# Kernel tuning notes

Measured on AMD Instinct MI355X. Metric: run time of the kernel, lower is better.

## Reference

```python
import jax, jax.numpy as jnp
import numpy as np

D = 256       # in_channels == hd_channels
H = 8         # heads
HC = D // H   # head dim = 32
NV = 30000    # variables
NC = 60000    # clauses
E = 120000    # edges per polarity


def setup_inputs() -> dict:
    key = jax.random.key(0)
    ks = jax.random.split(key, 16)
    std = 0.02
    v = jax.random.normal(ks[0], (NV, D), jnp.float32)
    c = jax.random.normal(ks[1], (NC, D), jnp.float32)
    # adj row0 indexes clauses (c), row1 indexes variables (v)
    adj_pos = jnp.stack([jax.random.randint(ks[2], (E,), 0, NC),
                         jax.random.randint(ks[3], (E,), 0, NV)]).astype(jnp.int32)
    adj_neg = jnp.stack([jax.random.randint(ks[4], (E,), 0, NC),
                         jax.random.randint(ks[5], (E,), 0, NV)]).astype(jnp.int32)
    # shared projections (ModuleList([lin]*2) shares one module)
    Wq = jax.random.normal(ks[6], (D, D), jnp.float32) * std
    bq = jnp.zeros((D,), jnp.float32)
    Wkv = jax.random.normal(ks[7], (D, 2 * D), jnp.float32) * std
    bkv = jnp.zeros((2 * D,), jnp.float32)
    ffn_v_w1 = jax.random.normal(ks[8], (D, D), jnp.float32) * std
    ffn_v_b1 = jnp.zeros((D,), jnp.float32)
    ffn_v_w2 = jax.random.normal(ks[9], (D, D), jnp.float32) * std
    ffn_v_b2 = jnp.zeros((D,), jnp.float32)
    ffn_c_w1 = jax.random.normal(ks[10], (D, D), jnp.float32) * std
    ffn_c_b1 = jnp.zeros((D,), jnp.float32)
    ffn_c_w2 = jax.random.normal(ks[11], (D, D), jnp.float32) * std
    ffn_c_b2 = jnp.zeros((D,), jnp.float32)
    ones = jnp.ones((D,), jnp.float32)
    zeros = jnp.zeros((D,), jnp.float32)
    return dict(v=v, c=c, adj_pos=adj_pos, adj_neg=adj_neg,
                Wq=Wq, bq=bq, Wkv=Wkv, bkv=bkv,
                ffn_v_w1=ffn_v_w1, ffn_v_b1=ffn_v_b1, ffn_v_w2=ffn_v_w2, ffn_v_b2=ffn_v_b2,
                ffn_c_w1=ffn_c_w1, ffn_c_b1=ffn_c_b1, ffn_c_w2=ffn_c_w2, ffn_c_b2=ffn_c_b2,
                ln_att_v_g=ones, ln_att_v_b=zeros, ln_ffn_v_g=ones, ln_ffn_v_b=zeros,
                ln_att_c_g=ones, ln_att_c_b=zeros, ln_ffn_c_g=ones, ln_ffn_c_b=zeros)


def _split(x):
    return x.reshape(x.shape[0], H, HC)


def _ln(x, g, b, eps=1e-5):
    m = jnp.mean(x, axis=-1, keepdims=True)
    va = jnp.mean(jnp.square(x - m), axis=-1, keepdims=True)
    return (x - m) * jax.lax.rsqrt(va + eps) * g + b


def _seg_softmax(x, seg, n):
    m = jax.ops.segment_max(x, seg, num_segments=n)      # (n, H)
    e = jnp.exp(x - m[seg])
    s = jax.ops.segment_sum(e, seg, num_segments=n)
    return e / s[seg]


def _sparse_attn(q, k, val, e_q, e_k, n_q):
    # q: (Lq,H,HC); k,val: (Lk,H,HC); per-edge dot -> segment softmax -> scatter aggregate
    qk = jnp.einsum('ehc,ehc->eh', q[e_q], k[e_k]) * (1.0 / np.sqrt(HC))
    alpha = _seg_softmax(qk, e_q, n_q)                   # (E,H)
    return jax.ops.segment_sum(alpha[:, :, None] * val[e_k], e_q, num_segments=n_q)


def _cross(x, y, adj, Wq, bq, Wkv, bkv):
    # adj[0] indexes y, adj[1] indexes x
    ey, ex = adj[0], adj[1]
    qx = _split(x @ Wq + bq)
    ky, vy = jnp.split(y @ Wkv + bkv, 2, axis=-1)
    w = _sparse_attn(qx, _split(ky), _split(vy), ex, ey, x.shape[0])   # x queries, transposed edges
    qy = _split(y @ Wq + bq)
    kx, vx = jnp.split(x @ Wkv + bkv, 2, axis=-1)
    u = _sparse_attn(qy, _split(kx), _split(vx), ey, ex, y.shape[0])   # y queries
    return w.reshape(x.shape[0], D), u.reshape(y.shape[0], D)


def _ffn(x, w1, b1, w2, b2):
    return jax.nn.gelu(x @ w1 + b1, approximate=False) @ w2 + b2


def reference(v, c, adj_pos, adj_neg, Wq, bq, Wkv, bkv,
              ffn_v_w1, ffn_v_b1, ffn_v_w2, ffn_v_b2,
              ffn_c_w1, ffn_c_b1, ffn_c_w2, ffn_c_b2,
              ln_att_v_g, ln_att_v_b, ln_ffn_v_g, ln_ffn_v_b,
              ln_att_c_g, ln_att_c_b, ln_ffn_c_g, ln_ffn_c_b):
    wp, up = _cross(v, c, adj_pos, Wq, bq, Wkv, bkv)
    wn, un = _cross(v, c, adj_neg, Wq, bq, Wkv, bkv)
    v1 = _ln(v + (wp + wn), ln_att_v_g, ln_att_v_b)
    c1 = _ln(c + (up + un), ln_att_c_g, ln_att_c_b)
    v2 = _ln(v1 + _ffn(v1, ffn_v_w1, ffn_v_b1, ffn_v_w2, ffn_v_b2), ln_ffn_v_g, ln_ffn_v_b)
    c2 = _ln(c1 + _ffn(c1, ffn_c_w1, ffn_c_b1, ffn_c_w2, ffn_c_b2), ln_ffn_c_g, ln_ffn_c_b)
    return (v2, c2)
```

## Files before the change

kernel.cpp:

```cpp
#include <hip/hip_runtime.h>
#include <math.h>

#define DD 256
#define NH 8

typedef __attribute__((ext_vector_type(8))) short short8;
typedef __attribute__((ext_vector_type(4))) float floatx4;

__device__ __forceinline__ float b2f(unsigned short u) {
    return __uint_as_float(((unsigned)u) << 16);
}
__device__ __forceinline__ unsigned short f2b(float f) {
    unsigned u = __float_as_uint(f);
    return (unsigned short)((u + 0x7fffu + ((u >> 16) & 1u)) >> 16);
}

__device__ __forceinline__ void gload_lds16(const void* g, void* l) {
    __builtin_amdgcn_global_load_lds(
        (const __attribute__((address_space(1))) void*)g,
        (__attribute__((address_space(3))) void*)l, 16, 0, 0);
}

__global__ void detect_dtype(const unsigned* __restrict__ ones_words, int* __restrict__ flag) {
    flag[0] = (ones_words[0] == 0x3F800000u) ? 0 : 1;
}

__device__ __forceinline__ void load8(const void* base, size_t off, int f32, unsigned short* dst) {
    if (f32) {
        const float4* p = (const float4*)((const float*)base + off);
        float4 x = p[0], y = p[1];
        dst[0] = f2b(x.x); dst[1] = f2b(x.y); dst[2] = f2b(x.z); dst[3] = f2b(x.w);
        dst[4] = f2b(y.x); dst[5] = f2b(y.y); dst[6] = f2b(y.z); dst[7] = f2b(y.w);
    } else {
        *(uint4*)dst = *(const uint4*)((const unsigned short*)base + off);
    }
}

__global__ void wt_build(const void* __restrict__ Wq, const void* __restrict__ Wkv,
                         const void* __restrict__ f1v, const void* __restrict__ f1c,
                         const void* __restrict__ f2v, const void* __restrict__ f2c,
                         short* __restrict__ wt, const int* __restrict__ flagp)
{
    const int extf = (*flagp == 0);
    const void* src; int N; size_t dst0;
    switch (blockIdx.z) {
        case 0:  src = Wq;  N = 256; dst0 = 0;          break;
        case 1:  src = Wkv; N = 512; dst0 = 256 * 256;  break;
        case 2:  src = f1v; N = 256; dst0 = 768 * 256;  break;
        case 3:  src = f1c; N = 256; dst0 = 1024 * 256; break;
        case 4:  src = f2v; N = 256; dst0 = 1280 * 256; break;
        default: src = f2c; N = 256; dst0 = 1536 * 256; break;
    }
    int n0 = blockIdx.x * 32, k0 = blockIdx.y * 32;
    if (n0 >= N) return;
    __shared__ short tile[32][33];
    int tx = threadIdx.x & 31, ty = threadIdx.x >> 5;
    #pragma unroll
    for (int i = 0; i < 32; i += 8) {
        int k = k0 + ty + i, n = n0 + tx;
        float val = extf ? ((const float*)src)[(size_t)k * N + n]
                         : b2f(((const unsigned short*)src)[(size_t)k * N + n]);
        tile[ty + i][tx] = (short)f2b(val);
    }
    __syncthreads();
    #pragma unroll
    for (int i = 0; i < 32; i += 8)
        wt[dst0 + (size_t)(n0 + ty + i) * 256 + k0 + tx] = tile[tx][ty + i];
}


__device__ __forceinline__ void stage_bchunk(const char* src32k, char* dst, int wave, int lane) {
    #pragma unroll
    for (int i = 0; i < 4; ++i) {
        int So = ((wave * 4 + i) << 10) + lane * 16;
        int Ls = So ^ (((So >> 9) & 7) << 4);
        gload_lds16(src32k + Ls, dst + ((wave * 4 + i) << 10));
    }
}

__device__ __forceinline__ short8 read_bfrag(const char* bbuf, int row, int bytecol) {
    int S = (row << 9) + bytecol;
    S ^= (row & 7) << 4;
    return *(const short8*)(bbuf + S);
}

__launch_bounds__(512)
__global__ void proj_gemm4(const void* __restrict__ va, const void* __restrict__ ca,
                           int NVr, int NCr, int bv,
                           const short* __restrict__ wt,
                           const void* __restrict__ bq, const void* __restrict__ bkv,
                           unsigned short* __restrict__ qbuf, unsigned short* __restrict__ kvbuf,
                           const int* __restrict__ flagp)
{
    __shared__ __align__(16) short As[128][264];
    __shared__ __align__(16) char Bs[2][64 * 512];
    const int extf = (*flagp == 0);
    const int t = threadIdx.x;
    const int wave = t >> 6, lane = t & 63;
    const int fr = lane & 15, fq = lane >> 4;
    const int bx = blockIdx.x;
    int grow0, nrows, abase_row; const void* asrc;
    if (bx < bv) { grow0 = bx * 128; asrc = va; abase_row = grow0; nrows = NVr - grow0; }
    else { int mc0 = (bx - bv) * 128; grow0 = NVr + mc0; asrc = ca; abase_row = mc0; nrows = NCr - mc0; }
    if (nrows > 128) nrows = 128;

    stage_bchunk((const char*)wt, Bs[0], wave, lane);
    {
        const int r = t >> 2, cb = (t & 3) * 8;
        #pragma unroll
        for (int cc = 0; cc < 8; ++cc) {
            int col = cb + cc * 32;
            __align__(16) unsigned short a8[8] = {0, 0, 0, 0, 0, 0, 0, 0};
            if (r < nrows) load8(asrc, (size_t)(abase_row + r) * DD + col, extf, a8);
            *(uint4*)(&As[r][col]) = *(const uint4*)a8;
        }
    }
    __syncthreads();

    int cur = 0;
    for (int nc = 0; nc < 12; ++nc) {
        if (nc + 1 < 12)
            stage_bchunk((const char*)(wt + (size_t)(nc + 1) * 64 * 256), Bs[cur ^ 1], wave, lane);
        floatx4 acc[4] = {};
        #pragma unroll
        for (int k8 = 0; k8 < 8; ++k8) {
            short8 af = *(const short8*)(&As[wave * 16 + fr][k8 * 32 + fq * 8]);
            short8 bf[4];
            #pragma unroll
            for (int j = 0; j < 4; ++j)
                bf[j] = read_bfrag(Bs[cur], j * 16 + fr, k8 * 64 + fq * 16);
            #pragma unroll
            for (int j = 0; j < 4; ++j)
                acc[j] = __builtin_amdgcn_mfma_f32_16x16x32_bf16(af, bf[j], acc[j], 0, 0, 0);
        }
        unsigned short* outp; int ldo, colbase; const void* bias;
        if (nc < 4) { outp = qbuf;  ldo = 256; colbase = nc * 64;       bias = bq;  }
        else        { outp = kvbuf; ldo = 512; colbase = (nc - 4) * 64; bias = bkv; }
        #pragma unroll
        for (int j = 0; j < 4; ++j) {
            int col = colbase + j * 16 + fr;
            float bvv = extf ? ((const float*)bias)[col] : b2f(((const unsigned short*)bias)[col]);
            #pragma unroll
            for (int r = 0; r < 4; ++r) {
                int rr = wave * 16 + fq * 4 + r;
                if (rr < nrows)
                    outp[(size_t)(grow0 + rr) * ldo + col] = f2b(acc[j][r] + bvv);
            }
        }
        __syncthreads();
        cur ^= 1;
    }
}

template<int EPI>
__launch_bounds__(512)
__global__ void ffn_gemm4(const unsigned short* __restrict__ A,
                          int NVr, int NCr, int bv,
                          const short* __restrict__ wtV, const short* __restrict__ wtC,
                          const void* __restrict__ biasV, const void* __restrict__ biasC,
                          void* __restrict__ outp, const int* __restrict__ flagp)
{
    __shared__ __align__(16) short As[128][264];
    __shared__ __align__(16) char Bs[2][64 * 512];
    const int extf = (*flagp == 0);
    const int t = threadIdx.x;
    const int wave = t >> 6, lane = t & 63;
    const int fr = lane & 15, fq = lane >> 4;
    const int bx = blockIdx.x;
    int grow0, nrows; const short* wtp; const void* bias;
    if (bx < bv) { grow0 = bx * 128; nrows = NVr - grow0; wtp = wtV; bias = biasV; }
    else { grow0 = NVr + (bx - bv) * 128; nrows = NVr + NCr - grow0; wtp = wtC; bias = biasC; }
    if (nrows > 128) nrows = 128;

    stage_bchunk((const char*)wtp, Bs[0], wave, lane);
    {
        const int r = t >> 2, cb = (t & 3) * 8;
        #pragma unroll
        for (int cc = 0; cc < 8; ++cc) {
            int col = cb + cc * 32;
            uint4 a8 = make_uint4(0u, 0u, 0u, 0u);
            if (r < nrows) a8 = *(const uint4*)(A + (size_t)(grow0 + r) * DD + col);
            *(uint4*)(&As[r][col]) = a8;
        }
    }
    __syncthreads();

    int cur = 0;
    for (int nc = 0; nc < 4; ++nc) {
        if (nc + 1 < 4)
            stage_bchunk((const char*)(wtp + (size_t)(nc + 1) * 64 * 256), Bs[cur ^ 1], wave, lane);
        floatx4 acc[4] = {};
        #pragma unroll
        for (int k8 = 0; k8 < 8; ++k8) {
            short8 af = *(const short8*)(&As[wave * 16 + fr][k8 * 32 + fq * 8]);
            short8 bf[4];
            #pragma unroll
            for (int j = 0; j < 4; ++j)
                bf[j] = read_bfrag(Bs[cur], j * 16 + fr, k8 * 64 + fq * 16);
            #pragma unroll
            for (int j = 0; j < 4; ++j)
                acc[j] = __builtin_amdgcn_mfma_f32_16x16x32_bf16(af, bf[j], acc[j], 0, 0, 0);
        }
        #pragma unroll
        for (int j = 0; j < 4; ++j) {
            int col = nc * 64 + j * 16 + fr;
            float bvv = extf ? ((const float*)bias)[col] : b2f(((const unsigned short*)bias)[col]);
            #pragma unroll
            for (int r = 0; r < 4; ++r) {
                int rr = wave * 16 + fq * 4 + r;
                if (rr < nrows) {
                    float x = acc[j][r] + bvv;
                    if (EPI == 1) {
                        x = 0.5f * x * (1.0f + erff(x * 0.70710678118654752f));
                        ((unsigned short*)outp)[(size_t)(grow0 + rr) * DD + col] = f2b(x);
                    } else {
                        ((float*)outp)[(size_t)(grow0 + rr) * DD + col] = x;
                    }
                }
            }
        }
        __syncthreads();
        cur ^= 1;
    }
}

__global__ void csr_count(const int* __restrict__ ap, const int* __restrict__ an,
                          int E, int NV, int NT, int* __restrict__ counts) {
    int e = blockIdx.x * 256 + threadIdx.x;
    if (e >= E) return;
    atomicAdd(&counts[ap[E + e]], 1);
    atomicAdd(&counts[NV + ap[e]], 1);
    atomicAdd(&counts[NT + an[E + e]], 1);
    atomicAdd(&counts[NT + NV + an[e]], 1);
}

__global__ void scan_block(const int* __restrict__ counts, int* __restrict__ offs,
                           int* __restrict__ bsum, int n) {
    __shared__ int sm[256];
    int i = blockIdx.x * 256 + threadIdx.x;
    int x = (i < n) ? counts[i] : 0;
    sm[threadIdx.x] = x;
    __syncthreads();
    #pragma unroll
    for (int d = 1; d < 256; d <<= 1) {
        int t = (threadIdx.x >= d) ? sm[threadIdx.x - d] : 0;
        __syncthreads();
        sm[threadIdx.x] += t;
        __syncthreads();
    }
    if (i < n) offs[i] = sm[threadIdx.x] - x;
    if (threadIdx.x == 255) bsum[blockIdx.x] = sm[255];
}

__global__ void scan_bsum(int* __restrict__ bsum, int nb) {
    __shared__ int sm[256];
    __shared__ int carry;
    if (threadIdx.x == 0) carry = 0;
    __syncthreads();
    for (int base = 0; base < nb; base += 256) {
        int i = base + threadIdx.x;
        int x = (i < nb) ? bsum[i] : 0;
        sm[threadIdx.x] = x;
        __syncthreads();
        #pragma unroll
        for (int d = 1; d < 256; d <<= 1) {
            int t = (threadIdx.x >= d) ? sm[threadIdx.x - d] : 0;
            __syncthreads();
            sm[threadIdx.x] += t;
            __syncthreads();
        }
        int excl = sm[threadIdx.x] - x + carry;
        if (i < nb) bsum[i] = excl;
        __syncthreads();
        if (threadIdx.x == 0) carry += sm[255];
        __syncthreads();
    }
}

__global__ void scan_add(int* __restrict__ offs, const int* __restrict__ bsum, int n) {
    int i = blockIdx.x * 256 + threadIdx.x;
    if (i < n) offs[i] += bsum[blockIdx.x];
}

__global__ void csr_fill(const int* __restrict__ ap, const int* __restrict__ an,
                         int E, int NV, int NT, int* __restrict__ offs, int* __restrict__ eids) {
    int e = blockIdx.x * 256 + threadIdx.x;
    if (e >= E) return;
    int p;
    p = atomicAdd(&offs[ap[E + e]], 1);            eids[p] = e * 2;
    p = atomicAdd(&offs[NV + ap[e]], 1);           eids[p] = e * 2 + 1;
    p = atomicAdd(&offs[NT + an[E + e]], 1);       eids[p] = e * 2;
    p = atomicAdd(&offs[NT + NV + an[e]], 1);      eids[p] = e * 2 + 1;
}

__launch_bounds__(256)
__global__ void edge_logits(const int* __restrict__ adj, int E, int NV,
                            const unsigned short* __restrict__ qbuf,
                            const unsigned short* __restrict__ kvbuf,
                            float* __restrict__ qk)
{
    int t = blockIdx.x * 256 + threadIdx.x;
    if (t >= E * 16) return;
    int e = t >> 4, rem = t & 15;
    int dir = rem >> 3, h = rem & 7;
    int ce = adj[e], xe = adj[E + e];
    int qrow = dir ? (NV + ce) : xe;
    int krow = dir ? xe : (NV + ce);
    const unsigned short* qp = qbuf + (size_t)qrow * DD + h * 32;
    const unsigned short* kp = kvbuf + (size_t)krow * 512 + h * 32;
    float s = 0.f;
    #pragma unroll
    for (int i = 0; i < 4; ++i) {
        uint4 qv = ((const uint4*)qp)[i];
        uint4 kv = ((const uint4*)kp)[i];
        const unsigned short* qa = (const unsigned short*)&qv;
        const unsigned short* ka = (const unsigned short*)&kv;
        #pragma unroll
        for (int j = 0; j < 8; ++j) s += b2f(qa[j]) * b2f(ka[j]);
    }
    qk[t] = s * 0.17677669529663689f;
}

__launch_bounds__(256)
__global__ void seg_attn(const int* __restrict__ offs_end, const int* __restrict__ counts,
                         const int* __restrict__ eids, const int* __restrict__ adj,
                         int E, int NV, const float* __restrict__ qk,
                         const unsigned short* __restrict__ kvbuf,
                         float* __restrict__ osum, int NT, int acc_mode)
{
    int seg = blockIdx.x * 4 + (threadIdx.x >> 6);
    if (seg >= NT) return;
    int lane = threadIdx.x & 63;
    int deg = counts[seg];
    float4* op = (float4*)(osum + (size_t)seg * DD) + lane;
    if (deg == 0) {
        if (!acc_mode) *op = make_float4(0.f, 0.f, 0.f, 0.f);
        return;
    }
    int beg = offs_end[seg] - deg;
    int slot = lane >> 3, h = lane & 7;
    float m = -1e30f;
    for (int j = slot; j < deg; j += 8)
        m = fmaxf(m, qk[(size_t)eids[beg + j] * 8 + h]);
    m = fmaxf(m, __shfl_xor(m, 8));
    m = fmaxf(m, __shfl_xor(m, 16));
    m = fmaxf(m, __shfl_xor(m, 32));
    float s = 0.f;
    for (int j = slot; j < deg; j += 8)
        s += __expf(qk[(size_t)eids[beg + j] * 8 + h] - m);
    s += __shfl_xor(s, 8);
    s += __shfl_xor(s, 16);
    s += __shfl_xor(s, 32);
    int h3 = lane >> 3;
    float m3 = __shfl(m, h3);
    float rs3 = 1.f / __shfl(s, h3);
    float a0 = 0.f, a1 = 0.f, a2 = 0.f, a3 = 0.f;
    for (int j = 0; j < deg; ++j) {
        int eid = eids[beg + j];
        int e = eid >> 1, dir = eid & 1;
        int krow = dir ? adj[E + e] : (NV + adj[e]);
        float alpha = __expf(qk[(size_t)eid * 8 + h3] - m3) * rs3;
        ushort4 vv = *(const ushort4*)(kvbuf + (size_t)krow * 512 + DD + lane * 4);
        a0 += alpha * b2f(vv.x);
        a1 += alpha * b2f(vv.y);
        a2 += alpha * b2f(vv.z);
        a3 += alpha * b2f(vv.w);
    }
    float4 o;
    if (acc_mode) {
        float4 old = *op;
        o.x = old.x + a0; o.y = old.y + a1; o.z = old.z + a2; o.w = old.w + a3;
    } else {
        o.x = a0; o.y = a1; o.z = a2; o.w = a3;
    }
    *op = o;
}

template<int BASE_EXT, int OUT_EXT>
__launch_bounds__(256)
__global__ void ln_res(const void* __restrict__ baseA, const void* __restrict__ baseB,
                       const float* __restrict__ add,
                       const void* __restrict__ gA, const void* __restrict__ bA,
                       const void* __restrict__ gB, const void* __restrict__ bB,
                       void* __restrict__ out, int NA, int Ntot, const int* __restrict__ flagp)
{
    int row = blockIdx.x * 4 + (threadIdx.x >> 6);
    if (row >= Ntot) return;
    int lane = threadIdx.x & 63;
    const int extf = (*flagp == 0);
    const void *base, *g, *b;
    size_t roff;
    if (row < NA) { base = baseA; g = gA; b = bA; roff = (size_t)row * DD; }
    else          { base = baseB; g = gB; b = bB; roff = (size_t)(row - NA) * DD; }
    float4 a = ((const float4*)(add + (size_t)row * DD))[lane];
    float y0, y1, y2, y3;
    if (BASE_EXT && extf) {
        float4 t = ((const float4*)((const float*)base + roff))[lane];
        y0 = t.x; y1 = t.y; y2 = t.z; y3 = t.w;
    } else {
        ushort4 t = ((const ushort4*)((const unsigned short*)base + roff))[lane];
        y0 = b2f(t.x); y1 = b2f(t.y); y2 = b2f(t.z); y3 = b2f(t.w);
    }
    y0 += a.x; y1 += a.y; y2 += a.z; y3 += a.w;
    float s = y0 + y1 + y2 + y3;
    #pragma unroll
    for (int off = 32; off; off >>= 1) s += __shfl_xor(s, off);
    float mean = s * (1.0f / DD);
    float d0 = y0 - mean, d1 = y1 - mean, d2 = y2 - mean, d3 = y3 - mean;
    float v = d0 * d0 + d1 * d1 + d2 * d2 + d3 * d3;
    #pragma unroll
    for (int off = 32; off; off >>= 1) v += __shfl_xor(v, off);
    float rstd = rsqrtf(v * (1.0f / DD) + 1e-5f);
    float g0, g1, g2, g3, t0, t1, t2, t3;
    if (extf) {
        float4 gg = ((const float4*)g)[lane]; float4 bt = ((const float4*)b)[lane];
        g0 = gg.x; g1 = gg.y; g2 = gg.z; g3 = gg.w;
        t0 = bt.x; t1 = bt.y; t2 = bt.z; t3 = bt.w;
    } else {
        ushort4 gg = ((const ushort4*)g)[lane]; ushort4 bt = ((const ushort4*)b)[lane];
        g0 = b2f(gg.x); g1 = b2f(gg.y); g2 = b2f(gg.z); g3 = b2f(gg.w);
        t0 = b2f(bt.x); t1 = b2f(bt.y); t2 = b2f(bt.z); t3 = b2f(bt.w);
    }
    float o0 = d0 * rstd * g0 + t0, o1 = d1 * rstd * g1 + t1;
    float o2 = d2 * rstd * g2 + t2, o3 = d3 * rstd * g3 + t3;
    if (OUT_EXT && extf) {
        float4 o; o.x = o0; o.y = o1; o.z = o2; o.w = o3;
        ((float4*)((float*)out + (size_t)row * DD))[lane] = o;
    } else {
        ushort4 o;
        o.x = f2b(o0); o.y = f2b(o1); o.z = f2b(o2); o.w = f2b(o3);
        ((ushort4*)((unsigned short*)out + (size_t)row * DD))[lane] = o;
    }
}

extern "C" void kernel_launch(void* const* d_in, const int* in_sizes, int n_in,
                              void* d_out, int out_size, void* d_ws, size_t ws_size,
                              hipStream_t stream)
{
    const void* v   = d_in[0];
    const void* c   = d_in[1];
    const int* adj_pos = (const int*)d_in[2];
    const int* adj_neg = (const int*)d_in[3];
    const void* Wq  = d_in[4];
    const void* bq  = d_in[5];
    const void* Wkv = d_in[6];
    const void* bkv = d_in[7];
    const void* fvw1 = d_in[8];
    const void* fvb1 = d_in[9];
    const void* fvw2 = d_in[10];
    const void* fvb2 = d_in[11];
    const void* fcw1 = d_in[12];
    const void* fcb1 = d_in[13];
    const void* fcw2 = d_in[14];
    const void* fcb2 = d_in[15];
    const void* lavg = d_in[16];
    const void* lavb = d_in[17];
    const void* lfvg = d_in[18];
    const void* lfvb = d_in[19];
    const void* lacg = d_in[20];
    const void* lacb = d_in[21];
    const void* lfcg = d_in[22];
    const void* lfcb = d_in[23];

    const int NV = in_sizes[0] / DD;
    const int NC = in_sizes[1] / DD;
    const int NT = NV + NC;
    const int E  = in_sizes[2] / 2;

    char* w = (char*)d_ws;
    int* flagp = (int*)w;
    size_t off = 256;
    float* osum = (float*)(w + off);
    off += (size_t)NT * DD * 4;
    unsigned short* qbuf = (unsigned short*)(w + off);
    off += (size_t)NT * DD * 2;
    unsigned short* kvbuf = (unsigned short*)(w + off);
    off += (size_t)NT * DD * 4;
    float* qkbuf = (float*)(w + off);
    off += (size_t)E * 16 * 4;
    int* counts = (int*)(w + off);
    off += (size_t)2 * NT * 4;
    int* offs = (int*)(w + off);
    off += (size_t)2 * NT * 4;
    int* eids = (int*)(w + off);
    off += (size_t)4 * E * 4;
    int* bsum = (int*)(w + off);
    off += 4096;
    short* wt = (short*)(w + off);

    dim3 blk(256), blk512(512);
    const int bv = (NV + 127) / 128, bc = (NC + 127) / 128;
    const int nbE = (E + 255) / 256;
    const int n2 = 2 * NT, nb2 = (n2 + 255) / 256;

    detect_dtype<<<dim3(1), dim3(1), 0, stream>>>((const unsigned*)lavg, flagp);
    wt_build<<<dim3(16, 8, 6), blk, 0, stream>>>(Wq, Wkv, fvw1, fcw1, fvw2, fcw2, wt, flagp);

    proj_gemm4<<<dim3(bv + bc), blk512, 0, stream>>>(v, c, NV, NC, bv, wt, bq, bkv,
                                                     qbuf, kvbuf, flagp);

    hipMemsetAsync(counts, 0, (size_t)n2 * 4, stream);
    csr_count<<<dim3(nbE), blk, 0, stream>>>(adj_pos, adj_neg, E, NV, NT, counts);
    scan_block<<<dim3(nb2), blk, 0, stream>>>(counts, offs, bsum, n2);
    scan_bsum<<<dim3(1), blk, 0, stream>>>(bsum, nb2);
    scan_add<<<dim3(nb2), blk, 0, stream>>>(offs, bsum, n2);
    csr_fill<<<dim3(nbE), blk, 0, stream>>>(adj_pos, adj_neg, E, NV, NT, offs, eids);

    for (int p = 0; p < 2; ++p) {
        const int* adj = p ? adj_neg : adj_pos;
        edge_logits<<<dim3((E * 16 + 255) / 256), blk, 0, stream>>>(adj, E, NV, qbuf, kvbuf, qkbuf);
        seg_attn<<<dim3((NT + 3) / 4), blk, 0, stream>>>(offs + (size_t)p * NT, counts + (size_t)p * NT,
                                                         eids, adj, E, NV, qkbuf, kvbuf, osum, NT, p);
    }

    unsigned short* x1 = qbuf;
    ln_res<1, 0><<<dim3((NT + 3) / 4), blk, 0, stream>>>(v, c, osum, lavg, lavb, lacg, lacb,
                                                         x1, NV, NT, flagp);

    unsigned short* hbuf = kvbuf;
    ffn_gemm4<1><<<dim3(bv + bc), blk512, 0, stream>>>(x1, NV, NC, bv,
                                                       wt + (size_t)768 * 256, wt + (size_t)1024 * 256,
                                                       fvb1, fcb1, hbuf, flagp);
    ffn_gemm4<2><<<dim3(bv + bc), blk512, 0, stream>>>(hbuf, NV, NC, bv,
                                                       wt + (size_t)1280 * 256, wt + (size_t)1536 * 256,
                                                       fvb2, fcb2, osum, flagp);

    ln_res<0, 1><<<dim3((NT + 3) / 4), blk, 0, stream>>>(x1, x1 + (size_t)NV * DD, osum,
                                                         lfvg, lfvb, lfcg, lfcb,
                                                         d_out, NV, NT, flagp);
}
```

Measured before the change: 803.0 us.

## Retile projection and FFN GEMMs to 2x4 wave grid with 256-wide N tiles

The projection and FFN GEMMs now stage B in 256-column by 64-k chunks and arrange the eight waves as a 2x4 grid. Each wave computes a 64x64 output tile with 4x4 MFMA accumulators instead of a 16x64 strip, so fragments are reused more and there are fewer LDS reads per MFMA. Launch bounds now request two blocks per CU. The cost is higher register pressure from 16 accumulator tiles, plus more barriers because there is a sync per k-substep.

```diff
diff --git a/kernel.cpp b/kernel.cpp
--- a/kernel.cpp
+++ b/kernel.cpp
@@ -69,23 +69,22 @@
 }
 
 
-__device__ __forceinline__ void stage_bchunk(const char* src32k, char* dst, int wave, int lane) {
+__device__ __forceinline__ void stage_b256(const short* wtp, int nbase, int ksub,
+                                           char* dstbuf, int wave, int lane)
+{
+    const char* wb = (const char*)wtp;
+    int b = lane & 7;
     #pragma unroll
     for (int i = 0; i < 4; ++i) {
-        int So = ((wave * 4 + i) << 10) + lane * 16;
-        int Ls = So ^ (((So >> 9) & 7) << 4);
-        gload_lds16(src32k + Ls, dst + ((wave * 4 + i) << 10));
-    }
-}
-
-__device__ __forceinline__ short8 read_bfrag(const char* bbuf, int row, int bytecol) {
-    int S = (row << 9) + bytecol;
-    S ^= (row & 7) << 4;
-    return *(const short8*)(bbuf + S);
-}
-
-__launch_bounds__(512)
-__global__ void proj_gemm4(const void* __restrict__ va, const void* __restrict__ ca,
+        int r = i * 64 + wave * 8 + (lane >> 3);
+        size_t src = (size_t)(nbase + r) * 512 + (size_t)ksub * 128
+                   + (size_t)((b * 16) ^ ((r & 7) << 4));
+        gload_lds16(wb + src, dstbuf + i * 8192 + wave * 1024);
+    }
+}
+
+__launch_bounds__(512, 2)
+__global__ void proj_gemm5(const void* __restrict__ va, const void* __restrict__ ca,
                            int NVr, int NCr, int bv,
                            const short* __restrict__ wt,
                            const void* __restrict__ bq, const void* __restrict__ bkv,
@@ -93,10 +92,11 @@
                            const int* __restrict__ flagp)
 {
     __shared__ __align__(16) short As[128][264];
-    __shared__ __align__(16) char Bs[2][64 * 512];
+    __shared__ __align__(16) char Bs[2][256 * 128];
     const int extf = (*flagp == 0);
     const int t = threadIdx.x;
     const int wave = t >> 6, lane = t & 63;
+    const int wm = wave >> 2, wn = wave & 3;
     const int fr = lane & 15, fq = lane >> 4;
     const int bx = blockIdx.x;
     int grow0, nrows, abase_row; const void* asrc;
@@ -104,67 +104,84 @@
     else { int mc0 = (bx - bv) * 128; grow0 = NVr + mc0; asrc = ca; abase_row = mc0; nrows = NCr - mc0; }
     if (nrows > 128) nrows = 128;
 
-    stage_bchunk((const char*)wt, Bs[0], wave, lane);
+    stage_b256(wt, 0, 0, Bs[0], wave, lane);
     {
-        const int r = t >> 2, cb = (t & 3) * 8;
-        #pragma unroll
-        for (int cc = 0; cc < 8; ++cc) {
-            int col = cb + cc * 32;
+        int rbase = t >> 3, cslot = t & 7;
+        #pragma unroll
+        for (int ii = 0; ii < 8; ++ii) {
+            int row = rbase + (ii >> 2) * 64;
+            int col = (cslot + (ii & 3) * 8) * 8;
             __align__(16) unsigned short a8[8] = {0, 0, 0, 0, 0, 0, 0, 0};
-            if (r < nrows) load8(asrc, (size_t)(abase_row + r) * DD + col, extf, a8);
-            *(uint4*)(&As[r][col]) = *(const uint4*)a8;
+            if (row < nrows) load8(asrc, (size_t)(abase_row + row) * DD + col, extf, a8);
+            *(uint4*)(&As[row][col]) = *(const uint4*)a8;
         }
     }
     __syncthreads();
 
     int cur = 0;
-    for (int nc = 0; nc < 12; ++nc) {
-        if (nc + 1 < 12)
-            stage_bchunk((const char*)(wt + (size_t)(nc + 1) * 64 * 256), Bs[cur ^ 1], wave, lane);
-        floatx4 acc[4] = {};
-        #pragma unroll
-        for (int k8 = 0; k8 < 8; ++k8) {
-            short8 af = *(const short8*)(&As[wave * 16 + fr][k8 * 32 + fq * 8]);
-            short8 bf[4];
+    for (int c = 0; c < 3; ++c) {
+        floatx4 acc[4][4] = {};
+        #pragma unroll
+        for (int s = 0; s < 4; ++s) {
+            int tt = c * 4 + s;
+            if (tt + 1 < 12)
+                stage_b256(wt, ((tt + 1) >> 2) * 256, (tt + 1) & 3, Bs[cur ^ 1], wave, lane);
+            const char* bcur = Bs[cur];
             #pragma unroll
-            for (int j = 0; j < 4; ++j)
-                bf[j] = read_bfrag(Bs[cur], j * 16 + fr, k8 * 64 + fq * 16);
-            #pragma unroll
-            for (int j = 0; j < 4; ++j)
-                acc[j] = __builtin_amdgcn_mfma_f32_16x16x32_bf16(af, bf[j], acc[j], 0, 0, 0);
-        }
-        unsigned short* outp; int ldo, colbase; const void* bias;
-        if (nc < 4) { outp = qbuf;  ldo = 256; colbase = nc * 64;       bias = bq;  }
-        else        { outp = kvbuf; ldo = 512; colbase = (nc - 4) * 64; bias = bkv; }
+            for (int k32 = 0; k32 < 2; ++k32) {
+                short8 afv[4], bfv[4];
+                #pragma unroll
+                for (int m = 0; m < 4; ++m)
+                    afv[m] = *(const short8*)(&As[wm * 64 + m * 16 + fr][s * 64 + k32 * 32 + fq * 8]);
+                #pragma unroll
+                for (int j = 0; j < 4; ++j) {
+                    int rn = wn * 64 + j * 16 + fr;
+                    int kb = (k32 * 64 + fq * 16) ^ ((rn & 7) << 4);
+                    bfv[j] = *(const short8*)(bcur + rn * 128 + kb);
+                }
+                #pragma unroll
+                for (int m = 0; m < 4; ++m)
+                    #pragma unroll
+                    for (int j = 0; j < 4; ++j)
+                        acc[m][j] = __builtin_amdgcn_mfma_f32_16x16x32_bf16(afv[m], bfv[j], acc[m][j], 0, 0, 0);
+            }
+            __syncthreads();
+            cur ^= 1;
+        }
+        unsigned short* outp; int ldo, colb; const void* bias;
+        if (c == 0) { outp = qbuf;  ldo = 256; colb = 0;             bias = bq;  }
+        else        { outp = kvbuf; ldo = 512; colb = (c - 1) * 256; bias = bkv; }
         #pragma unroll
         for (int j = 0; j < 4; ++j) {
-            int col = colbase + j * 16 + fr;
+            int col = colb + wn * 64 + j * 16 + fr;
             float bvv = extf ? ((const float*)bias)[col] : b2f(((const unsigned short*)bias)[col]);
             #pragma unroll
-            for (int r = 0; r < 4; ++r) {
-                int rr = wave * 16 + fq * 4 + r;
-                if (rr < nrows)
-                    outp[(size_t)(grow0 + rr) * ldo + col] = f2b(acc[j][r] + bvv);
+            for (int m = 0; m < 4; ++m) {
+                #pragma unroll
+                for (int r = 0; r < 4; ++r) {
+                    int rr = wm * 64 + m * 16 + fq * 4 + r;
+                    if (rr < nrows)
+                        outp[(size_t)(grow0 + rr) * ldo + col] = f2b(acc[m][j][r] + bvv);
+                }
             }
         }
-        __syncthreads();
-        cur ^= 1;
     }
 }
 
 template<int EPI>
-__launch_bounds__(512)
-__global__ void ffn_gemm4(const unsigned short* __restrict__ A,
+__launch_bounds__(512, 2)
+__global__ void ffn_gemm5(const unsigned short* __restrict__ A,
                           int NVr, int NCr, int bv,
                           const short* __restrict__ wtV, const short* __restrict__ wtC,
                           const void* __restrict__ biasV, const void* __restrict__ biasC,
                           void* __restrict__ outp, const int* __restrict__ flagp)
 {
     __shared__ __align__(16) short As[128][264];
-    __shared__ __align__(16) char Bs[2][64 * 512];
+    __shared__ __align__(16) char Bs[2][256 * 128];
     const int extf = (*flagp == 0);
     const int t = threadIdx.x;
     const int wave = t >> 6, lane = t & 63;
+    const int wm = wave >> 2, wn = wave & 3;
     const int fr = lane & 15, fq = lane >> 4;
     const int bx = blockIdx.x;
     int grow0, nrows; const short* wtp; const void* bias;
@@ -172,44 +189,59 @@
     else { grow0 = NVr + (bx - bv) * 128; nrows = NVr + NCr - grow0; wtp = wtC; bias = biasC; }
     if (nrows > 128) nrows = 128;
 
-    stage_bchunk((const char*)wtp, Bs[0], wave, lane);
+    stage_b256(wtp, 0, 0, Bs[0], wave, lane);
     {
-        const int r = t >> 2, cb = (t & 3) * 8;
-        #pragma unroll
-        for (int cc = 0; cc < 8; ++cc) {
-            int col = cb + cc * 32;
+        int rbase = t >> 3, cslot = t & 7;
+        #pragma unroll
+        for (int ii = 0; ii < 8; ++ii) {
+            int row = rbase + (ii >> 2) * 64;
+            int col = (cslot + (ii & 3) * 8) * 8;
             uint4 a8 = make_uint4(0u, 0u, 0u, 0u);
-            if (r < nrows) a8 = *(const uint4*)(A + (size_t)(grow0 + r) * DD + col);
-            *(uint4*)(&As[r][col]) = a8;
+            if (row < nrows) a8 = *(const uint4*)(A + (size_t)(grow0 + row) * DD + col);
+            *(uint4*)(&As[row][col]) = a8;
         }
     }
     __syncthreads();
 
     int cur = 0;
-    for (int nc = 0; nc < 4; ++nc) {
-        if (nc + 1 < 4)
-            stage_bchunk((const char*)(wtp + (size_t)(nc + 1) * 64 * 256), Bs[cur ^ 1], wave, lane);
-        floatx4 acc[4] = {};
-        #pragma unroll
-        for (int k8 = 0; k8 < 8; ++k8) {
-            short8 af = *(const short8*)(&As[wave * 16 + fr][k8 * 32 + fq * 8]);
-            short8 bf[4];
+    floatx4 acc[4][4] = {};
+    #pragma unroll
+    for (int s = 0; s < 4; ++s) {
+        if (s + 1 < 4)
+            stage_b256(wtp, 0, s + 1, Bs[cur ^ 1], wave, lane);
+        const char* bcur = Bs[cur];
+        #pragma unroll
+        for (int k32 = 0; k32 < 2; ++k32) {
+            short8 afv[4], bfv[4];
             #pragma unroll
-            for (int j = 0; j < 4; ++j)
-                bf[j] = read_bfrag(Bs[cur], j * 16 + fr, k8 * 64 + fq * 16);
+            for (int m = 0; m < 4; ++m)
+                afv[m] = *(const short8*)(&As[wm * 64 + m * 16 + fr][s * 64 + k32 * 32 + fq * 8]);
             #pragma unroll
-            for (int j = 0; j < 4; ++j)
-                acc[j] = __builtin_amdgcn_mfma_f32_16x16x32_bf16(af, bf[j], acc[j], 0, 0, 0);
-        }
-        #pragma unroll
-        for (int j = 0; j < 4; ++j) {
-            int col = nc * 64 + j * 16 + fr;
-            float bvv = extf ? ((const float*)bias)[col] : b2f(((const unsigned short*)bias)[col]);
+            for (int j = 0; j < 4; ++j) {
+                int rn = wn * 64 + j * 16 + fr;
+                int kb = (k32 * 64 + fq * 16) ^ ((rn & 7) << 4);
+                bfv[j] = *(const short8*)(bcur + rn * 128 + kb);
+            }
+            #pragma unroll
+            for (int m = 0; m < 4; ++m)
+                #pragma unroll
+                for (int j = 0; j < 4; ++j)
+                    acc[m][j] = __builtin_amdgcn_mfma_f32_16x16x32_bf16(afv[m], bfv[j], acc[m][j], 0, 0, 0);
+        }
+        __syncthreads();
+        cur ^= 1;
+    }
+    #pragma unroll
+    for (int j = 0; j < 4; ++j) {
+        int col = wn * 64 + j * 16 + fr;
+        float bvv = extf ? ((const float*)bias)[col] : b2f(((const unsigned short*)bias)[col]);
+        #pragma unroll
+        for (int m = 0; m < 4; ++m) {
             #pragma unroll
             for (int r = 0; r < 4; ++r) {
-                int rr = wave * 16 + fq * 4 + r;
+                int rr = wm * 64 + m * 16 + fq * 4 + r;
                 if (rr < nrows) {
-                    float x = acc[j][r] + bvv;
+                    float x = acc[m][j][r] + bvv;
                     if (EPI == 1) {
                         x = 0.5f * x * (1.0f + erff(x * 0.70710678118654752f));
                         ((unsigned short*)outp)[(size_t)(grow0 + rr) * DD + col] = f2b(x);
@@ -219,8 +251,6 @@
                 }
             }
         }
-        __syncthreads();
-        cur ^= 1;
     }
 }
 
@@ -496,7 +526,7 @@
     detect_dtype<<<dim3(1), dim3(1), 0, stream>>>((const unsigned*)lavg, flagp);
     wt_build<<<dim3(16, 8, 6), blk, 0, stream>>>(Wq, Wkv, fvw1, fcw1, fvw2, fcw2, wt, flagp);
 
-    proj_gemm4<<<dim3(bv + bc), blk512, 0, stream>>>(v, c, NV, NC, bv, wt, bq, bkv,
+    proj_gemm5<<<dim3(bv + bc), blk512, 0, stream>>>(v, c, NV, NC, bv, wt, bq, bkv,
                                                      qbuf, kvbuf, flagp);
 
     hipMemsetAsync(counts, 0, (size_t)n2 * 4, stream);
@@ -518,10 +548,10 @@
                                                          x1, NV, NT, flagp);
 
     unsigned short* hbuf = kvbuf;
-    ffn_gemm4<1><<<dim3(bv + bc), blk512, 0, stream>>>(x1, NV, NC, bv,
+    ffn_gemm5<1><<<dim3(bv + bc), blk512, 0, stream>>>(x1, NV, NC, bv,
                                                        wt + (size_t)768 * 256, wt + (size_t)1024 * 256,
                                                        fvb1, fcb1, hbuf, flagp);
-    ffn_gemm4<2><<<dim3(bv + bc), blk512, 0, stream>>>(hbuf, NV, NC, bv,
+    ffn_gemm5<2><<<dim3(bv + bc), blk512, 0, stream>>>(hbuf, NV, NC, bv,
                                                        wt + (size_t)1280 * 256, wt + (size_t)1536 * 256,
                                                        fvb2, fcb2, osum, flagp);
 
```

Result: faster. 754.1 us (-6.1%).
